# Optimization experiments

Hardware: AMD Instinct MI355X
Metric: run time of the kernel (lower is better)

## Reference

```python
import jax, jax.numpy as jnp
import numpy as np

N, BSZ, NE, DIN, DH, RH = 32, 512, 7, 512, 256, 64
NPAIR = NE * (NE - 1) // 2  # 21
PAIRS = [(i, j) for i in range(NE) for j in range(i + 1, NE)]


def setup_inputs() -> dict:
    key = jax.random.key(0)
    ks = jax.random.split(key, 16)
    def w(k, shape, fan_in):
        return jax.random.normal(k, shape, jnp.float32) / np.sqrt(fan_in)
    return {
        "input": jax.random.normal(ks[0], (N, BSZ, NE, DIN), jnp.float32),
        "ctx_differences": jax.random.normal(ks[1], (BSZ, NPAIR, 5), jnp.float32),
        "lang_input": jax.random.normal(ks[2], (N, BSZ, 128), jnp.float32),
        "num_markables": jax.random.randint(ks[3], (BSZ,), 0, N),
        # unary feedforward: 2 hidden layers + output layer (output_dim=2)
        "W0": w(ks[4], (DIN, DH), DIN), "b0": jnp.zeros((DH,), jnp.float32),
        "W1": w(ks[5], (DH, DH), DH), "b1": jnp.zeros((DH,), jnp.float32),
        "W2": w(ks[6], (DH, 2), DH), "b2": jnp.zeros((2,), jnp.float32),
        # relation encoder: 1 hidden layer (dim 64), output 3
        "R0": w(ks[7], (5, RH), 5), "r0": jnp.zeros((RH,), jnp.float32),
        "R1": w(ks[8], (RH, 3), RH), "r1": jnp.zeros((3,), jnp.float32),
    }


def reference(input, ctx_differences, lang_input, num_markables,
              W0, b0, W1, b1, W2, b2, R0, r0, R1, r1):
    # unary potentials: [N, bsz, 7, 2]
    h = jax.nn.relu(input @ W0 + b0)
    h = jax.nn.relu(h @ W1 + b1)
    un = h @ W2 + b2
    # binary potentials: [bsz, 21, 3] -> map to 2x2 via fixed matrix
    h2 = jax.nn.relu(ctx_differences @ R0 + r0)
    bp3 = h2 @ R1 + r1
    Mmap = jnp.array([[1, 0, 0], [0, 1, 0], [0, 1, 0], [0, 0, 1]], jnp.float32)
    bp4 = jnp.einsum('bpx,yx->bpy', bp3, Mmap).reshape(BSZ, NPAIR, 2, 2)

    # accumulate log-factors into the joint log tensor [N, bsz, 2,...,2]
    joint = jnp.zeros((N, BSZ) + (2,) * NE, jnp.float32)
    for i in range(NE):
        shp = [N, BSZ] + [1] * NE
        shp[2 + i] = 2
        joint = joint + un[:, :, i].reshape(shp)
    for p, (i, j) in enumerate(PAIRS):
        shp = [1, BSZ] + [1] * NE
        shp[2 + i] = 2
        shp[2 + j] = 2
        joint = joint + bp4[:, p].reshape(shp)

    # marginals: logsumexp over all entity axes but one -> [N, bsz, 7, 2]
    ent_axes = tuple(range(2, 2 + NE))
    marg = jnp.stack(
        [jax.scipy.special.logsumexp(joint, axis=tuple(a for a in ent_axes if a != 2 + i))
         for i in range(NE)], axis=2)
    lm = jax.nn.log_softmax(marg, axis=-1)
    marginal_log_probs = lm[..., 1] - lm[..., 0]  # [N, bsz, 7]

    jf = joint.reshape(N, BSZ, 2 ** NE)
    joint_log_probs = jax.nn.log_softmax(jf, axis=-1).reshape((N, BSZ) + (2,) * NE)
    return (marginal_log_probs, joint_log_probs)
```

## Files before the change

### kernel.cpp

```cpp
#include <hip/hip_runtime.h>

typedef __bf16 bf16;
typedef bf16 bf16x8 __attribute__((ext_vector_type(8)));
typedef bf16 bf16x4 __attribute__((ext_vector_type(4)));
typedef float f32x4 __attribute__((ext_vector_type(4)));

#define MFMA(a, b, c) __builtin_amdgcn_mfma_f32_16x16x32_bf16((a), (b), (c), 0, 0, 0)


__global__ __launch_bounds__(256) void k_prep_bsum(
    const float* __restrict__ W0, const float* __restrict__ W1,
    const float* __restrict__ W2, bf16* __restrict__ W0f,
    bf16* __restrict__ W1f, bf16* __restrict__ W2f,
    const float* __restrict__ ctx, const float* __restrict__ R0,
    const float* __restrict__ r0, const float* __restrict__ R1,
    const float* __restrict__ r1, float* __restrict__ bsum) {
  if (blockIdx.x < 98) {
    int g = blockIdx.x * 256 + threadIdx.x;
    if (g < 16384) {
      int mt = g >> 10, ks = (g >> 6) & 15, lane = g & 63;
      int m = mt * 16 + (lane & 15);
      int kb = ks * 32 + (lane >> 4) * 8;
      bf16x8 v;
#pragma unroll
      for (int j = 0; j < 8; ++j) v[j] = (bf16)W0[(kb + j) * 256 + m];
      *(bf16x8*)&W0f[g * 8] = v;
    } else if (g < 24576) {
      int h = g - 16384;
      int mt = h >> 9, ks = (h >> 6) & 7, lane = h & 63;
      int m = mt * 16 + (lane & 15);
      int kb = ks * 32 + (lane >> 4) * 8;
      bf16x8 v;
#pragma unroll
      for (int j = 0; j < 8; ++j) v[j] = (bf16)W1[(kb + j) * 256 + m];
      *(bf16x8*)&W1f[h * 8] = v;
    } else {
      int h = g - 24576;
      int ks = h >> 6, lane = h & 63;
      int c = lane & 15;
      int kb = ks * 32 + (lane >> 4) * 8;
      bf16x8 v;
#pragma unroll
      for (int j = 0; j < 8; ++j) v[j] = (c < 2) ? (bf16)W2[(kb + j) * 2 + c] : (bf16)0.0f;
      *(bf16x8*)&W2f[h * 8] = v;
    }
  } else {
    __shared__ float ctx_l[105], R0_l[320], r0_l[64], R1_l[192], r1_l[3];
    __shared__ float h2[21 * 65];
    __shared__ float bp[63];
    const int t = threadIdx.x;
    const int b = blockIdx.x - 98;
    if (t < 105) ctx_l[t] = ctx[b * 105 + t];
    if (t < 64) r0_l[t] = r0[t];
    if (t < 192) R1_l[t] = R1[t];
    if (t < 3) r1_l[t] = r1[t];
    for (int i = t; i < 320; i += 256) R0_l[i] = R0[i];
    __syncthreads();
    for (int idx = t; idx < 1344; idx += 256) {
      int p = idx >> 6, u = idx & 63;
      float a = r0_l[u];
#pragma unroll
      for (int x = 0; x < 5; ++x) a += ctx_l[p * 5 + x] * R0_l[x * 64 + u];
      h2[p * 65 + u] = fmaxf(a, 0.f);
    }
    __syncthreads();
    if (t < 63) {
      int p = t / 3, y = t - p * 3;
      float a = r1_l[y];
      for (int u = 0; u < 64; ++u) a += h2[p * 65 + u] * R1_l[u * 3 + y];
      bp[t] = a;
    }
    __syncthreads();
    if (t < 128) {
      float a = 0.f;
      int pi = 0;
#pragma unroll
      for (int i = 0; i < 7; ++i)
#pragma unroll
        for (int j = i + 1; j < 7; ++j) {
          int bi = (t >> (6 - i)) & 1, bj = (t >> (6 - j)) & 1;
          a += bp[pi * 3 + bi + bj];
          ++pi;
        }
      bsum[b * 128 + t] = a;
    }
  }
}

__global__ __launch_bounds__(256, 3) void k_unary(const float* __restrict__ input,
                                                  const bf16* __restrict__ W0f,
                                                  const bf16* __restrict__ W1f,
                                                  const bf16* __restrict__ W2f,
                                                  const float* __restrict__ b0,
                                                  const float* __restrict__ b1,
                                                  const float* __restrict__ b2,
                                                  float* __restrict__ un) {
  __shared__ bf16 inp_lds[64 * 68];
  __shared__ bf16 h_lds[64 * 264];
  __shared__ float bias_lds[512];
  __shared__ float part_lds[512];

  const int tid = threadIdx.x;
  const int wave = tid >> 6;
  const int lane = tid & 63;
  const int l16 = lane & 15;
  const int lq = lane >> 4;
  const long m0 = (long)blockIdx.x * 64;

  bias_lds[tid] = b0[tid];
  bias_lds[256 + tid] = b1[tid];

  f32x4 acc[4][4];
#pragma unroll
  for (int i = 0; i < 4; ++i)
#pragma unroll
    for (int j = 0; j < 4; ++j) acc[i][j] = (f32x4){0.f, 0.f, 0.f, 0.f};

  const int r = tid >> 2;
  const int q = tid & 3;
  const float* gp = input + (m0 + r) * 512 + q * 16;
  float4 x0 = ((const float4*)gp)[0];
  float4 x1 = ((const float4*)gp)[1];
  float4 x2 = ((const float4*)gp)[2];
  float4 x3 = ((const float4*)gp)[3];

  for (int it = 0; it < 8; ++it) {
    __syncthreads();
    bf16x8 wlo, whi;
    wlo[0] = (bf16)x0.x; wlo[1] = (bf16)x0.y; wlo[2] = (bf16)x0.z; wlo[3] = (bf16)x0.w;
    wlo[4] = (bf16)x1.x; wlo[5] = (bf16)x1.y; wlo[6] = (bf16)x1.z; wlo[7] = (bf16)x1.w;
    whi[0] = (bf16)x2.x; whi[1] = (bf16)x2.y; whi[2] = (bf16)x2.z; whi[3] = (bf16)x2.w;
    whi[4] = (bf16)x3.x; whi[5] = (bf16)x3.y; whi[6] = (bf16)x3.z; whi[7] = (bf16)x3.w;
    *(bf16x8*)&inp_lds[r * 68 + q * 16] = wlo;
    *(bf16x8*)&inp_lds[r * 68 + q * 16 + 8] = whi;
    __syncthreads();
    if (it < 7) {
      gp += 64;
      x0 = ((const float4*)gp)[0];
      x1 = ((const float4*)gp)[1];
      x2 = ((const float4*)gp)[2];
      x3 = ((const float4*)gp)[3];
    }
#pragma unroll
    for (int s = 0; s < 2; ++s) {
      bf16x8 bfr[4];
#pragma unroll
      for (int nt = 0; nt < 4; ++nt)
        bfr[nt] = *(const bf16x8*)&inp_lds[(nt * 16 + l16) * 68 + s * 32 + lq * 8];
#pragma unroll
      for (int mt = 0; mt < 4; ++mt) {
        bf16x8 a = *(const bf16x8*)&W0f[(((wave * 4 + mt) * 16 + it * 2 + s) * 64 + lane) * 8];
#pragma unroll
        for (int nt = 0; nt < 4; ++nt) acc[mt][nt] = MFMA(a, bfr[nt], acc[mt][nt]);
      }
    }
  }

#pragma unroll
  for (int mt = 0; mt < 4; ++mt) {
    const int nbase = (wave * 4 + mt) * 16 + lq * 4;
    float bb[4];
#pragma unroll
    for (int g = 0; g < 4; ++g) bb[g] = bias_lds[nbase + g];
#pragma unroll
    for (int nt = 0; nt < 4; ++nt) {
      const int m = nt * 16 + l16;
      bf16x4 hv;
#pragma unroll
      for (int g = 0; g < 4; ++g) hv[g] = (bf16)fmaxf(acc[mt][nt][g] + bb[g], 0.f);
      *(bf16x4*)&h_lds[m * 264 + nbase] = hv;
    }
  }
  __syncthreads();

#pragma unroll
  for (int i = 0; i < 4; ++i)
#pragma unroll
    for (int j = 0; j < 4; ++j) acc[i][j] = (f32x4){0.f, 0.f, 0.f, 0.f};
#pragma unroll
  for (int ks = 0; ks < 8; ++ks) {
    bf16x8 bfr[4];
#pragma unroll
    for (int nt = 0; nt < 4; ++nt)
      bfr[nt] = *(const bf16x8*)&h_lds[(nt * 16 + l16) * 264 + ks * 32 + lq * 8];
#pragma unroll
    for (int mt = 0; mt < 4; ++mt) {
      bf16x8 a = *(const bf16x8*)&W1f[(((wave * 4 + mt) * 8 + ks) * 64 + lane) * 8];
#pragma unroll
      for (int nt = 0; nt < 4; ++nt) acc[mt][nt] = MFMA(a, bfr[nt], acc[mt][nt]);
    }
  }
  __syncthreads();

#pragma unroll
  for (int mt = 0; mt < 4; ++mt) {
    const int nbase = (wave * 4 + mt) * 16 + lq * 4;
    float bb[4];
#pragma unroll
    for (int g = 0; g < 4; ++g) bb[g] = bias_lds[256 + nbase + g];
#pragma unroll
    for (int nt = 0; nt < 4; ++nt) {
      const int m = nt * 16 + l16;
      bf16x4 hv;
#pragma unroll
      for (int g = 0; g < 4; ++g) hv[g] = (bf16)fmaxf(acc[mt][nt][g] + bb[g], 0.f);
      *(bf16x4*)&h_lds[m * 264 + nbase] = hv;
    }
  }
  __syncthreads();

  f32x4 acc2[4];
#pragma unroll
  for (int i = 0; i < 4; ++i) acc2[i] = (f32x4){0.f, 0.f, 0.f, 0.f};
#pragma unroll
  for (int s = 0; s < 2; ++s) {
    const int ks = wave * 2 + s;
    bf16x8 a = *(const bf16x8*)&W2f[(ks * 64 + lane) * 8];
#pragma unroll
    for (int nt = 0; nt < 4; ++nt) {
      bf16x8 b = *(const bf16x8*)&h_lds[(nt * 16 + l16) * 264 + ks * 32 + lq * 8];
      acc2[nt] = MFMA(a, b, acc2[nt]);
    }
  }
  if (lane < 16) {
#pragma unroll
    for (int nt = 0; nt < 4; ++nt) {
      part_lds[((wave * 4 + nt) * 16 + lane) * 2 + 0] = acc2[nt][0];
      part_lds[((wave * 4 + nt) * 16 + lane) * 2 + 1] = acc2[nt][1];
    }
  }
  __syncthreads();
  if (tid < 128) {
    const int mloc = tid >> 1, c = tid & 1;
    const int nt = mloc >> 4, l = mloc & 15;
    float s = b2[c];
#pragma unroll
    for (int w2 = 0; w2 < 4; ++w2) s += part_lds[((w2 * 4 + nt) * 16 + l) * 2 + c];
    un[(m0 + mloc) * 2 + c] = s;
  }
}

__global__ __launch_bounds__(256) void k_joint(const float* __restrict__ un,
                                               const float* __restrict__ bsum,
                                               float* __restrict__ out_marg,
                                               float* __restrict__ out_joint) {
  const int lane = threadIdx.x & 63;
  const int wave = threadIdx.x >> 6;
  const int gw = blockIdx.x * 4 + wave;
  const int b = gw & 511;
  const long row = gw;
  const int urow = __builtin_amdgcn_readfirstlane(gw);
  float u[14];
#pragma unroll
  for (int i = 0; i < 14; ++i) u[i] = un[(long)urow * 14 + i];
  const float bs0 = bsum[b * 128 + lane];
  const float bs1 = bsum[b * 128 + 64 + lane];
  float jc = 0.f;
#pragma unroll
  for (int i = 1; i < 7; ++i) jc += u[i * 2 + ((lane >> (6 - i)) & 1)];
  const float j0 = bs0 + jc + u[0];
  const float j1 = bs1 + jc + u[1];
  float m = fmaxf(j0, j1);
#pragma unroll
  for (int o = 1; o < 64; o <<= 1) m = fmaxf(m, __shfl_xor(m, o, 64));
  const float e0 = __expf(j0 - m), e1 = __expf(j1 - m);
  float t = e0 + e1;
  float s1e = e1;
  float uu[6];
#pragma unroll
  for (int q = 0; q < 6; ++q) {
    float pt = __shfl_xor(t, 1 << q, 64);
    uu[q] = ((lane >> q) & 1) ? t : pt;
    t += pt;
    s1e += __shfl_xor(s1e, 1 << q, 64);
#pragma unroll
    for (int jq = 0; jq < q; ++jq) uu[jq] += __shfl_xor(uu[jq], 1 << q, 64);
  }
  const float lZ = m + __logf(t);
  out_joint[row * 128 + lane] = j0 - lZ;
  out_joint[row * 128 + 64 + lane] = j1 - lZ;
  if (lane < 7) {
    const float s1 = (lane == 0) ? s1e : uu[6 - lane];
    out_marg[row * 7 + lane] = __logf(s1) - __logf(t - s1);
  }
}

extern "C" void kernel_launch(void* const* d_in, const int* in_sizes, int n_in,
                              void* d_out, int out_size, void* d_ws, size_t ws_size,
                              hipStream_t stream) {
  const float* input = (const float*)d_in[0];
  const float* ctx   = (const float*)d_in[1];
  const float* W0 = (const float*)d_in[4];
  const float* b0 = (const float*)d_in[5];
  const float* W1 = (const float*)d_in[6];
  const float* b1 = (const float*)d_in[7];
  const float* W2 = (const float*)d_in[8];
  const float* b2 = (const float*)d_in[9];
  const float* R0 = (const float*)d_in[10];
  const float* r0 = (const float*)d_in[11];
  const float* R1 = (const float*)d_in[12];
  const float* r1 = (const float*)d_in[13];

  char* ws = (char*)d_ws;
  bf16* W0f  = (bf16*)(ws + 0);
  bf16* W1f  = (bf16*)(ws + 262144);
  bf16* W2f  = (bf16*)(ws + 393216);
  float* un  = (float*)(ws + 401408);
  float* bsm = (float*)(ws + 1318912);

  float* out_marg = (float*)d_out;
  float* out_joint = out_marg + 114688;

  hipLaunchKernelGGL(k_prep_bsum, dim3(610), dim3(256), 0, stream,
                     W0, W1, W2, W0f, W1f, W2f, ctx, R0, r0, R1, r1, bsm);
  hipLaunchKernelGGL(k_unary, dim3(1792), dim3(256), 0, stream,
                     input, W0f, W1f, W2f, b0, b1, b2, un);
  hipLaunchKernelGGL(k_joint, dim3(4096), dim3(256), 0, stream, un, bsm, out_marg, out_joint);
}
```

Measured before the change: 409.4 us.

## Split unary MLP into layer-0 GEMM and fused layer-1/2 kernel with double-buffered tiles

Replaces the single fused unary MLP kernel with two kernels. The first computes layer 0 on 128x128 tiles, with LDS double-buffering of both input and weights, and writes a bf16 hidden activation to workspace. The second computes layer 1 and folds the 256->2 output layer into an fp32 epilogue using shuffle reductions, which removes the padded W2 MFMA path. The aim is better operand reuse and load/compute overlap than the old 64-row tiles that streamed weights from global memory. The cost is an extra global round-trip of the roughly 58 MB hidden activation and one more kernel launch.

Result: no change. 416.8 us (+1.8%).

```diff
diff --git a/kernel.cpp b/kernel.cpp
--- a/kernel.cpp
+++ b/kernel.cpp
@@ -2,7 +2,6 @@
 
 typedef __bf16 bf16;
 typedef bf16 bf16x8 __attribute__((ext_vector_type(8)));
-typedef bf16 bf16x4 __attribute__((ext_vector_type(4)));
 typedef float f32x4 __attribute__((ext_vector_type(4)));
 
 #define MFMA(a, b, c) __builtin_amdgcn_mfma_f32_16x16x32_bf16((a), (b), (c), 0, 0, 0)
@@ -10,46 +9,36 @@
 
 __global__ __launch_bounds__(256) void k_prep_bsum(
     const float* __restrict__ W0, const float* __restrict__ W1,
-    const float* __restrict__ W2, bf16* __restrict__ W0f,
-    bf16* __restrict__ W1f, bf16* __restrict__ W2f,
+    bf16* __restrict__ W0B, bf16* __restrict__ W1B,
     const float* __restrict__ ctx, const float* __restrict__ R0,
     const float* __restrict__ r0, const float* __restrict__ R1,
     const float* __restrict__ r1, float* __restrict__ bsum) {
-  if (blockIdx.x < 98) {
+  if (blockIdx.x < 96) {
     int g = blockIdx.x * 256 + threadIdx.x;
     if (g < 16384) {
-      int mt = g >> 10, ks = (g >> 6) & 15, lane = g & 63;
-      int m = mt * 16 + (lane & 15);
-      int kb = ks * 32 + (lane >> 4) * 8;
+      int l = g & 63;
+      int n = ((g >> 10) << 4) + (l & 15);
+      int kb = (((g >> 6) & 15) << 5) + ((l >> 4) << 3);
       bf16x8 v;
 #pragma unroll
-      for (int j = 0; j < 8; ++j) v[j] = (bf16)W0[(kb + j) * 256 + m];
-      *(bf16x8*)&W0f[g * 8] = v;
-    } else if (g < 24576) {
+      for (int j = 0; j < 8; ++j) v[j] = (bf16)W0[(kb + j) * 256 + n];
+      *(bf16x8*)&W0B[g * 8] = v;
+    } else {
       int h = g - 16384;
-      int mt = h >> 9, ks = (h >> 6) & 7, lane = h & 63;
-      int m = mt * 16 + (lane & 15);
-      int kb = ks * 32 + (lane >> 4) * 8;
+      int l = h & 63;
+      int n = ((h >> 9) << 4) + (l & 15);
+      int kb = (((h >> 6) & 7) << 5) + ((l >> 4) << 3);
       bf16x8 v;
 #pragma unroll
-      for (int j = 0; j < 8; ++j) v[j] = (bf16)W1[(kb + j) * 256 + m];
-      *(bf16x8*)&W1f[h * 8] = v;
-    } else {
-      int h = g - 24576;
-      int ks = h >> 6, lane = h & 63;
-      int c = lane & 15;
-      int kb = ks * 32 + (lane >> 4) * 8;
-      bf16x8 v;
-#pragma unroll
-      for (int j = 0; j < 8; ++j) v[j] = (c < 2) ? (bf16)W2[(kb + j) * 2 + c] : (bf16)0.0f;
-      *(bf16x8*)&W2f[h * 8] = v;
+      for (int j = 0; j < 8; ++j) v[j] = (bf16)W1[(kb + j) * 256 + n];
+      *(bf16x8*)&W1B[h * 8] = v;
     }
   } else {
     __shared__ float ctx_l[105], R0_l[320], r0_l[64], R1_l[192], r1_l[3];
     __shared__ float h2[21 * 65];
     __shared__ float bp[63];
     const int t = threadIdx.x;
-    const int b = blockIdx.x - 98;
+    const int b = blockIdx.x - 96;
     if (t < 105) ctx_l[t] = ctx[b * 105 + t];
     if (t < 64) r0_l[t] = r0[t];
     if (t < 192) R1_l[t] = R1[t];
@@ -87,28 +76,22 @@
   }
 }
 
-__global__ __launch_bounds__(256, 3) void k_unary(const float* __restrict__ input,
-                                                  const bf16* __restrict__ W0f,
-                                                  const bf16* __restrict__ W1f,
-                                                  const bf16* __restrict__ W2f,
-                                                  const float* __restrict__ b0,
-                                                  const float* __restrict__ b1,
-                                                  const float* __restrict__ b2,
-                                                  float* __restrict__ un) {
-  __shared__ bf16 inp_lds[64 * 68];
-  __shared__ bf16 h_lds[64 * 264];
-  __shared__ float bias_lds[512];
-  __shared__ float part_lds[512];
-
+__global__ __launch_bounds__(256, 3) void k_l0(const float* __restrict__ X,
+                                               const bf16* __restrict__ W0B,
+                                               const float* __restrict__ b0,
+                                               bf16* __restrict__ h0) {
+  __shared__ __align__(16) float xs[2][128 * 36];
+  __shared__ __align__(16) bf16 wsb[2][8 * 64 * 8];
   const int tid = threadIdx.x;
-  const int wave = tid >> 6;
-  const int lane = tid & 63;
-  const int l16 = lane & 15;
-  const int lq = lane >> 4;
-  const long m0 = (long)blockIdx.x * 64;
-
-  bias_lds[tid] = b0[tid];
-  bias_lds[256 + tid] = b1[tid];
+  const int w = tid >> 6, lane = tid & 63, l16 = lane & 15, quad = lane >> 4;
+  const int mb = blockIdx.x >> 1, nb = blockIdx.x & 1;
+  const int mt0 = (w >> 1) * 4;
+  const int nt0 = (w & 1) * 4;
+
+  const int xr = tid >> 1, xh = tid & 1;
+  const float* xg = X + (long)(mb * 128 + xr) * 512 + xh * 16;
+  const int ws0 = tid * 2;
+  const int wnt = ws0 >> 6, wl = ws0 & 63;
 
   f32x4 acc[4][4];
 #pragma unroll
@@ -116,127 +99,176 @@
 #pragma unroll
     for (int j = 0; j < 4; ++j) acc[i][j] = (f32x4){0.f, 0.f, 0.f, 0.f};
 
-  const int r = tid >> 2;
-  const int q = tid & 3;
-  const float* gp = input + (m0 + r) * 512 + q * 16;
-  float4 x0 = ((const float4*)gp)[0];
-  float4 x1 = ((const float4*)gp)[1];
-  float4 x2 = ((const float4*)gp)[2];
-  float4 x3 = ((const float4*)gp)[3];
+  float4 xv0 = ((const float4*)xg)[0], xv1 = ((const float4*)xg)[1];
+  float4 xv2 = ((const float4*)xg)[2], xv3 = ((const float4*)xg)[3];
+  int4 wv0 = *(const int4*)&W0B[(((nb * 8 + wnt) * 16) * 64 + wl) * 8];
+  int4 wv1 = *(const int4*)&W0B[(((nb * 8 + wnt) * 16) * 64 + wl + 1) * 8];
+  {
+    float* xd = &xs[0][xr * 36 + xh * 16];
+    *(float4*)xd = xv0; *(float4*)(xd + 4) = xv1;
+    *(float4*)(xd + 8) = xv2; *(float4*)(xd + 12) = xv3;
+    *(int4*)&wsb[0][ws0 * 8] = wv0; *(int4*)&wsb[0][(ws0 + 1) * 8] = wv1;
+  }
+  __syncthreads();
+
+  for (int it = 0; it < 16; ++it) {
+    const int cur = it & 1;
+    if (it < 15) {
+      const float* xp = xg + (it + 1) * 32;
+      xv0 = ((const float4*)xp)[0]; xv1 = ((const float4*)xp)[1];
+      xv2 = ((const float4*)xp)[2]; xv3 = ((const float4*)xp)[3];
+      wv0 = *(const int4*)&W0B[(((nb * 8 + wnt) * 16 + it + 1) * 64 + wl) * 8];
+      wv1 = *(const int4*)&W0B[(((nb * 8 + wnt) * 16 + it + 1) * 64 + wl + 1) * 8];
+    }
+    bf16x8 af[4], bf[4];
+#pragma unroll
+    for (int mt = 0; mt < 4; ++mt) {
+      const float* ap = &xs[cur][((mt0 + mt) * 16 + l16) * 36 + quad * 8];
+      f32x4 a0 = *(const f32x4*)ap;
+      f32x4 a1 = *(const f32x4*)(ap + 4);
+      bf16x8 t;
+      t[0] = (bf16)a0[0]; t[1] = (bf16)a0[1]; t[2] = (bf16)a0[2]; t[3] = (bf16)a0[3];
+      t[4] = (bf16)a1[0]; t[5] = (bf16)a1[1]; t[6] = (bf16)a1[2]; t[7] = (bf16)a1[3];
+      af[mt] = t;
+    }
+#pragma unroll
+    for (int nt = 0; nt < 4; ++nt)
+      bf[nt] = *(const bf16x8*)&wsb[cur][((nt0 + nt) * 64 + lane) * 8];
+#pragma unroll
+    for (int mt = 0; mt < 4; ++mt)
+#pragma unroll
+      for (int nt = 0; nt < 4; ++nt) acc[mt][nt] = MFMA(af[mt], bf[nt], acc[mt][nt]);
+    if (it < 15) {
+      float* xd = &xs[cur ^ 1][xr * 36 + xh * 16];
+      *(float4*)xd = xv0; *(float4*)(xd + 4) = xv1;
+      *(float4*)(xd + 8) = xv2; *(float4*)(xd + 12) = xv3;
+      *(int4*)&wsb[cur ^ 1][ws0 * 8] = wv0; *(int4*)&wsb[cur ^ 1][(ws0 + 1) * 8] = wv1;
+      __syncthreads();
+    }
+  }
+
+  float bb[4];
+#pragma unroll
+  for (int nt = 0; nt < 4; ++nt) bb[nt] = b0[nb * 128 + (nt0 + nt) * 16 + l16];
+  __syncthreads();
+  bf16* hs = (bf16*)&xs[0][0];
+#pragma unroll
+  for (int mt = 0; mt < 4; ++mt)
+#pragma unroll
+    for (int nt = 0; nt < 4; ++nt)
+#pragma unroll
+      for (int r = 0; r < 4; ++r)
+        hs[((mt0 + mt) * 16 + quad * 4 + r) * 136 + (nt0 + nt) * 16 + l16] =
+            (bf16)fmaxf(acc[mt][nt][r] + bb[nt], 0.f);
+  __syncthreads();
+  const long gb = (long)(mb * 128 + xr) * 256 + nb * 128 + xh * 64;
+  const bf16* hr = &hs[xr * 136 + xh * 64];
+#pragma unroll
+  for (int c = 0; c < 8; ++c)
+    *(int4*)&h0[gb + c * 8] = *(const int4*)&hr[c * 8];
+}
+
+__global__ __launch_bounds__(512, 4) void k_l12(const bf16* __restrict__ h0,
+                                                const bf16* __restrict__ W1B,
+                                                const float* __restrict__ b1,
+                                                const float* __restrict__ W2,
+                                                const float* __restrict__ b2,
+                                                float* __restrict__ un) {
+  __shared__ __align__(16) bf16 as2[2][128 * 40];
+  __shared__ __align__(16) bf16 wsb[2][16 * 64 * 8];
+  __shared__ float b1s[256];
+  __shared__ float w2s[512];
+  __shared__ float parts[2][128][2];
+  const int tid = threadIdx.x;
+  const int w = tid >> 6, lane = tid & 63, l16 = lane & 15, quad = lane >> 4;
+  const int mb = blockIdx.x;
+  const int mt0 = (w >> 1) * 2;
+  const int ntq = (w & 1) * 8;
+  if (tid < 256) b1s[tid] = b1[tid];
+  w2s[tid] = W2[tid & 511];
+
+  const int ar = tid >> 2, aq = tid & 3;
+  const bf16* ag = h0 + (long)(mb * 128 + ar) * 256 + aq * 8;
+  const int ws0 = tid * 2;
+  const int wnt = ws0 >> 6, wl = ws0 & 63;
+
+  f32x4 acc[2][8];
+#pragma unroll
+  for (int i = 0; i < 2; ++i)
+#pragma unroll
+    for (int j = 0; j < 8; ++j) acc[i][j] = (f32x4){0.f, 0.f, 0.f, 0.f};
+
+  int4 av = *(const int4*)ag;
+  int4 wv0 = *(const int4*)&W1B[((wnt * 8) * 64 + wl) * 8];
+  int4 wv1 = *(const int4*)&W1B[((wnt * 8) * 64 + wl + 1) * 8];
+  *(int4*)&as2[0][ar * 40 + aq * 8] = av;
+  *(int4*)&wsb[0][ws0 * 8] = wv0; *(int4*)&wsb[0][(ws0 + 1) * 8] = wv1;
+  __syncthreads();
 
   for (int it = 0; it < 8; ++it) {
-    __syncthreads();
-    bf16x8 wlo, whi;
-    wlo[0] = (bf16)x0.x; wlo[1] = (bf16)x0.y; wlo[2] = (bf16)x0.z; wlo[3] = (bf16)x0.w;
-    wlo[4] = (bf16)x1.x; wlo[5] = (bf16)x1.y; wlo[6] = (bf16)x1.z; wlo[7] = (bf16)x1.w;
-    whi[0] = (bf16)x2.x; whi[1] = (bf16)x2.y; whi[2] = (bf16)x2.z; whi[3] = (bf16)x2.w;
-    whi[4] = (bf16)x3.x; whi[5] = (bf16)x3.y; whi[6] = (bf16)x3.z; whi[7] = (bf16)x3.w;
-    *(bf16x8*)&inp_lds[r * 68 + q * 16] = wlo;
-    *(bf16x8*)&inp_lds[r * 68 + q * 16 + 8] = whi;
-    __syncthreads();
+    const int cur = it & 1;
     if (it < 7) {
-      gp += 64;
-      x0 = ((const float4*)gp)[0];
-      x1 = ((const float4*)gp)[1];
-      x2 = ((const float4*)gp)[2];
-      x3 = ((const float4*)gp)[3];
-    }
-#pragma unroll
-    for (int s = 0; s < 2; ++s) {
-      bf16x8 bfr[4];
+      av = *(const int4*)(ag + (it + 1) * 32);
+      wv0 = *(const int4*)&W1B[((wnt * 8 + it + 1) * 64 + wl) * 8];
+      wv1 = *(const int4*)&W1B[((wnt * 8 + it + 1) * 64 + wl + 1) * 8];
+    }
+    bf16x8 af[2];
+#pragma unroll
+    for (int mt = 0; mt < 2; ++mt)
+      af[mt] = *(const bf16x8*)&as2[cur][((mt0 + mt) * 16 + l16) * 40 + quad * 8];
+#pragma unroll
+    for (int h = 0; h < 2; ++h) {
+      bf16x8 bf[4];
 #pragma unroll
       for (int nt = 0; nt < 4; ++nt)
-        bfr[nt] = *(const bf16x8*)&inp_lds[(nt * 16 + l16) * 68 + s * 32 + lq * 8];
-#pragma unroll
-      for (int mt = 0; mt < 4; ++mt) {
-        bf16x8 a = *(const bf16x8*)&W0f[(((wave * 4 + mt) * 16 + it * 2 + s) * 64 + lane) * 8];
-#pragma unroll
-        for (int nt = 0; nt < 4; ++nt) acc[mt][nt] = MFMA(a, bfr[nt], acc[mt][nt]);
+        bf[nt] = *(const bf16x8*)&wsb[cur][((ntq + h * 4 + nt) * 64 + lane) * 8];
+#pragma unroll
+      for (int mt = 0; mt < 2; ++mt)
+#pragma unroll
+        for (int nt = 0; nt < 4; ++nt)
+          acc[mt][h * 4 + nt] = MFMA(af[mt], bf[nt], acc[mt][h * 4 + nt]);
+    }
+    if (it < 7) {
+      *(int4*)&as2[cur ^ 1][ar * 40 + aq * 8] = av;
+      *(int4*)&wsb[cur ^ 1][ws0 * 8] = wv0; *(int4*)&wsb[cur ^ 1][(ws0 + 1) * 8] = wv1;
+      __syncthreads();
+    }
+  }
+
+  float sv[16];
+#pragma unroll
+  for (int i = 0; i < 16; ++i) sv[i] = 0.f;
+#pragma unroll
+  for (int nt = 0; nt < 8; ++nt) {
+    const int n = (ntq + nt) * 16 + l16;
+    const float bias = b1s[n];
+    const float w2a = w2s[n * 2], w2b = w2s[n * 2 + 1];
+#pragma unroll
+    for (int mt = 0; mt < 2; ++mt)
+#pragma unroll
+      for (int r = 0; r < 4; ++r) {
+        const float h1 = fmaxf(acc[mt][nt][r] + bias, 0.f);
+        sv[(mt * 4 + r) * 2 + 0] += h1 * w2a;
+        sv[(mt * 4 + r) * 2 + 1] += h1 * w2b;
       }
-    }
-  }
-
-#pragma unroll
-  for (int mt = 0; mt < 4; ++mt) {
-    const int nbase = (wave * 4 + mt) * 16 + lq * 4;
-    float bb[4];
-#pragma unroll
-    for (int g = 0; g < 4; ++g) bb[g] = bias_lds[nbase + g];
-#pragma unroll
-    for (int nt = 0; nt < 4; ++nt) {
-      const int m = nt * 16 + l16;
-      bf16x4 hv;
-#pragma unroll
-      for (int g = 0; g < 4; ++g) hv[g] = (bf16)fmaxf(acc[mt][nt][g] + bb[g], 0.f);
-      *(bf16x4*)&h_lds[m * 264 + nbase] = hv;
-    }
-  }
-  __syncthreads();
-
-#pragma unroll
-  for (int i = 0; i < 4; ++i)
-#pragma unroll
-    for (int j = 0; j < 4; ++j) acc[i][j] = (f32x4){0.f, 0.f, 0.f, 0.f};
-#pragma unroll
-  for (int ks = 0; ks < 8; ++ks) {
-    bf16x8 bfr[4];
-#pragma unroll
-    for (int nt = 0; nt < 4; ++nt)
-      bfr[nt] = *(const bf16x8*)&h_lds[(nt * 16 + l16) * 264 + ks * 32 + lq * 8];
-#pragma unroll
-    for (int mt = 0; mt < 4; ++mt) {
-      bf16x8 a = *(const bf16x8*)&W1f[(((wave * 4 + mt) * 8 + ks) * 64 + lane) * 8];
-#pragma unroll
-      for (int nt = 0; nt < 4; ++nt) acc[mt][nt] = MFMA(a, bfr[nt], acc[mt][nt]);
-    }
-  }
-  __syncthreads();
-
-#pragma unroll
-  for (int mt = 0; mt < 4; ++mt) {
-    const int nbase = (wave * 4 + mt) * 16 + lq * 4;
-    float bb[4];
-#pragma unroll
-    for (int g = 0; g < 4; ++g) bb[g] = bias_lds[256 + nbase + g];
-#pragma unroll
-    for (int nt = 0; nt < 4; ++nt) {
-      const int m = nt * 16 + l16;
-      bf16x4 hv;
-#pragma unroll
-      for (int g = 0; g < 4; ++g) hv[g] = (bf16)fmaxf(acc[mt][nt][g] + bb[g], 0.f);
-      *(bf16x4*)&h_lds[m * 264 + nbase] = hv;
-    }
-  }
-  __syncthreads();
-
-  f32x4 acc2[4];
-#pragma unroll
-  for (int i = 0; i < 4; ++i) acc2[i] = (f32x4){0.f, 0.f, 0.f, 0.f};
-#pragma unroll
-  for (int s = 0; s < 2; ++s) {
-    const int ks = wave * 2 + s;
-    bf16x8 a = *(const bf16x8*)&W2f[(ks * 64 + lane) * 8];
-#pragma unroll
-    for (int nt = 0; nt < 4; ++nt) {
-      bf16x8 b = *(const bf16x8*)&h_lds[(nt * 16 + l16) * 264 + ks * 32 + lq * 8];
-      acc2[nt] = MFMA(a, b, acc2[nt]);
-    }
-  }
-  if (lane < 16) {
-#pragma unroll
-    for (int nt = 0; nt < 4; ++nt) {
-      part_lds[((wave * 4 + nt) * 16 + lane) * 2 + 0] = acc2[nt][0];
-      part_lds[((wave * 4 + nt) * 16 + lane) * 2 + 1] = acc2[nt][1];
-    }
-  }
-  __syncthreads();
-  if (tid < 128) {
-    const int mloc = tid >> 1, c = tid & 1;
-    const int nt = mloc >> 4, l = mloc & 15;
-    float s = b2[c];
-#pragma unroll
-    for (int w2 = 0; w2 < 4; ++w2) s += part_lds[((w2 * 4 + nt) * 16 + l) * 2 + c];
-    un[(m0 + mloc) * 2 + c] = s;
+  }
+#pragma unroll
+  for (int i = 0; i < 16; ++i)
+#pragma unroll
+    for (int o = 1; o < 16; o <<= 1) sv[i] += __shfl_xor(sv[i], o, 64);
+  if (l16 == 0) {
+#pragma unroll
+    for (int mt = 0; mt < 2; ++mt)
+#pragma unroll
+      for (int r = 0; r < 4; ++r)
+#pragma unroll
+        for (int c = 0; c < 2; ++c)
+          parts[w & 1][(mt0 + mt) * 16 + quad * 4 + r][c] = sv[(mt * 4 + r) * 2 + c];
+  }
+  __syncthreads();
+  if (tid < 256) {
+    const int m = tid >> 1, c = tid & 1;
+    un[(long)(mb * 128 + m) * 2 + c] = parts[0][m][c] + parts[1][m][c] + b2[c];
   }
 }
 
@@ -302,18 +334,18 @@
   const float* r1 = (const float*)d_in[13];
 
   char* ws = (char*)d_ws;
-  bf16* W0f  = (bf16*)(ws + 0);
-  bf16* W1f  = (bf16*)(ws + 262144);
-  bf16* W2f  = (bf16*)(ws + 393216);
-  float* un  = (float*)(ws + 401408);
-  float* bsm = (float*)(ws + 1318912);
+  bf16* W0B = (bf16*)(ws + 0);
+  bf16* W1B = (bf16*)(ws + 262144);
+  bf16* h0  = (bf16*)(ws + 393216);
+  float* un  = (float*)(ws + 59113472);
+  float* bsm = (float*)(ws + 60030976);
 
   float* out_marg = (float*)d_out;
   float* out_joint = out_marg + 114688;
 
-  hipLaunchKernelGGL(k_prep_bsum, dim3(610), dim3(256), 0, stream,
-                     W0, W1, W2, W0f, W1f, W2f, ctx, R0, r0, R1, r1, bsm);
-  hipLaunchKernelGGL(k_unary, dim3(1792), dim3(256), 0, stream,
-                     input, W0f, W1f, W2f, b0, b1, b2, un);
+  hipLaunchKernelGGL(k_prep_bsum, dim3(608), dim3(256), 0, stream,
+                     W0, W1, W0B, W1B, ctx, R0, r0, R1, r1, bsm);
+  hipLaunchKernelGGL(k_l0, dim3(1792), dim3(256), 0, stream, input, W0B, b0, h0);
+  hipLaunchKernelGGL(k_l12, dim3(896), dim3(512), 0, stream, h0, W1B, b1, W2, b2, un);
   hipLaunchKernelGGL(k_joint, dim3(4096), dim3(256), 0, stream, un, bsm, out_marg, out_joint);
 }
```
